# Kernel optimization log

Measured on AMD Instinct MI355X. Metric: run time of the kernel, lower is better.

The kernel has to match this reference:

```python
import jax, jax.numpy as jnp
import numpy as np
from jax import lax

SIGMA = 1.0
SIGMA_CUTOFF = 2.0
TAU = 1.0
EPS = 1e-6


def _gauss_kernel1d(sigma=SIGMA, cutoff=SIGMA_CUTOFF):
    r = int(round(cutoff * sigma))
    x = np.arange(-r, r + 1, dtype=np.float32)
    k = np.exp(-(x ** 2) / (2.0 * sigma ** 2))
    return jnp.asarray(k / k.sum())


def _smooth3d(x, k1d):
    # x: [1, 3, D, H, W]; separable depthwise Gaussian along each spatial axis
    k = k1d.shape[0]
    for axis in range(3):
        shape = [1, 1, 1]
        shape[axis] = k
        w = jnp.broadcast_to(k1d.reshape(shape), (3, 1) + tuple(shape))  # [3,1,kd,kh,kw]
        x = lax.conv_general_dilated(
            x, w, window_strides=(1, 1, 1), padding='SAME',
            feature_group_count=3,
            dimension_numbers=('NCDHW', 'OIDHW', 'NCDHW'))
    return x


def setup_inputs() -> dict:
    key = jax.random.key(0)
    k1, k2 = jax.random.split(key)
    shape = (1, 1, 128, 160, 160)
    moving_image = jax.random.normal(k1, shape, dtype=jnp.float32)
    fixed_image = jax.random.normal(k2, shape, dtype=jnp.float32)
    return {"moving_image": moving_image, "fixed_image": fixed_image, "iterations": 10}


def reference(moving_image, fixed_image, iterations):
    mov = moving_image[0, 0]  # [D,H,W]
    fix = fixed_image[0, 0]
    D, H, W = mov.shape
    dtype = mov.dtype
    grid = jnp.stack(jnp.meshgrid(
        jnp.arange(D, dtype=dtype),
        jnp.arange(H, dtype=dtype),
        jnp.arange(W, dtype=dtype), indexing='ij'))  # [3,D,H,W]
    grad_fixed = jnp.stack(jnp.gradient(fix))  # [3,D,H,W] (passive gradient, precomputed)
    k1d = _gauss_kernel1d()

    def warp(vf):
        coords = grid + vf
        return jax.scipy.ndimage.map_coordinates(
            mov, [coords[0], coords[1], coords[2]], order=1, mode='constant', cval=0.0)

    def step(vf, _):
        warped = warp(vf)                      # trilinear spatial transformer
        diff = warped - fix                    # intensity difference
        grad_warped = jnp.stack(jnp.gradient(warped))
        g = grad_warped + grad_fixed           # 'dual' demons gradient
        denom = jnp.sum(g * g, axis=0) + diff * diff
        scale = jnp.where(denom > EPS, -diff / denom, 0.0)  # demon force magnitude
        forces = scale[None] * g               # [3,D,H,W]
        vf = vf + TAU * forces                 # vector-field update
        vf = _smooth3d(vf[None], k1d)[0]       # Gaussian regularization
        return vf, None

    vf0 = jnp.zeros((3, D, H, W), dtype=dtype)
    vf, _ = lax.scan(step, vf0, None, length=iterations)
    return vf[None]  # [1,3,D,H,W]
```

## Files before the change

kernel.cpp:

```cpp
#include <hip/hip_runtime.h>
#include <math.h>

#define D_ 128
#define H_ 160
#define W_ 160
#define NVOX (D_*H_*W_)
#define HW (H_*W_)
#define N4 (NVOX/4)
#define HW4 (HW/4)

#define K0 0.40261996f
#define K1 0.24420134f
#define K2 0.05448868f

union F4 { float4 v; float a[4]; };

__device__ __forceinline__ float4 zero4() { float4 z; z.x=z.y=z.z=z.w=0.f; return z; }
__device__ __forceinline__ float4 bcast4(float x) { float4 r; r.x=r.y=r.z=r.w=x; return r; }

#define GLOAD_LDS16(g, l) __builtin_amdgcn_global_load_lds( \
    (const __attribute__((address_space(1))) void*)(g), \
    (__attribute__((address_space(3))) void*)(l), 16, 0, 0)

__device__ __forceinline__ float fetch_mov(const float* __restrict__ m, int d, int h, int w) {
    if ((unsigned)d >= (unsigned)D_ || (unsigned)h >= (unsigned)H_ || (unsigned)w >= (unsigned)W_) return 0.0f;
    return m[(size_t)(d*H_ + h)*W_ + w];
}

__device__ __forceinline__ float trilerp(const float* __restrict__ mov,
                                         float cd, float ch, float cw) {
    float fd = floorf(cd), fh = floorf(ch), fw = floorf(cw);
    int di = (int)fd, hi = (int)fh, wi = (int)fw;
    float td = cd - fd, th = ch - fh, tw = cw - fw;
    float c000, c001, c010, c011, c100, c101, c110, c111;
    if (di >= 0 && di < D_-1 && hi >= 0 && hi < H_-1 && wi >= 0 && wi < W_-1) {
        const float* p = mov + (size_t)di*HW + hi*W_ + wi;
        c000 = p[0];    c001 = p[1];
        c010 = p[W_];   c011 = p[W_+1];
        const float* q = p + HW;
        c100 = q[0];    c101 = q[1];
        c110 = q[W_];   c111 = q[W_+1];
    } else {
        c000 = fetch_mov(mov, di,   hi,   wi  );
        c001 = fetch_mov(mov, di,   hi,   wi+1);
        c010 = fetch_mov(mov, di,   hi+1, wi  );
        c011 = fetch_mov(mov, di,   hi+1, wi+1);
        c100 = fetch_mov(mov, di+1, hi,   wi  );
        c101 = fetch_mov(mov, di+1, hi,   wi+1);
        c110 = fetch_mov(mov, di+1, hi+1, wi  );
        c111 = fetch_mov(mov, di+1, hi+1, wi+1);
    }
    float c00 = c000 + tw*(c001 - c000);
    float c01 = c010 + tw*(c011 - c010);
    float c10 = c100 + tw*(c101 - c100);
    float c11 = c110 + tw*(c111 - c110);
    float c0 = c00 + th*(c01 - c00);
    float c1 = c10 + th*(c11 - c10);
    return c0 + td*(c1 - c0);
}

#define UROW 48

__global__ __launch_bounds__(256, 4) void force_wh_kernel(const float* __restrict__ warped,
                                                          const float* __restrict__ fix,
                                                          const float* __restrict__ vf,
                                                          float* __restrict__ tout,
                                                          int zero_vf) {
    __shared__ float u[3][36][UROW];
    __shared__ float tw[38][48];
    __shared__ float tf[38][48];
    const int tx = threadIdx.x;
    const int ty = threadIdx.y;
    const int tid = ty*8 + tx;
    const int bswz = (blockIdx.x & 7)*400 + (blockIdx.x >> 3);
    const int d   = bswz / 25;
    const int rem = bswz % 25;
    const int h0 = (rem / 5) * 32;
    const int w0 = (rem % 5) * 32;

    #define UF4(ch, r, fc) (((float4*)&u[(ch)][(r)][0]) + ((fc) ^ ((r)&3)))

    {
        const float* wplane = warped + (size_t)d*HW;
        const float* fplane = fix    + (size_t)d*HW;
        #pragma unroll
        for (int k = 0; k < 2; ++k) {
            int s = (k == 0) ? tid : 200 + tid;
            int R  = s / 12, C4 = s % 12;
            int gh = h0 - 3 + R;
            int ghc = gh < 0 ? 0 : (gh > H_-1 ? H_-1 : gh);
            int gw = w0 - 8 + 4*C4;
            int gwc = gw < 0 ? 0 : (gw > W_-4 ? W_-4 : gw);
            const float* ws2 = wplane + (size_t)ghc*W_ + gwc;
            const float* fs2 = fplane + (size_t)ghc*W_ + gwc;
            GLOAD_LDS16(ws2, ((float4*)tw) + s);
            GLOAD_LDS16(fs2, ((float4*)tf) + s);
        }
    }
    __syncthreads();
    if (w0 == 0 || w0 == 128) {
        if (tid < 152) {
            int vol = tid / 76;
            int t2  = tid % 76;
            int R = t2 / 2, C = t2 % 2;
            float (*tp)[48] = vol ? tf : tw;
            int dstc = (w0 == 0) ? C : (10 + C);
            int srcf = (w0 == 0) ? 8 : 39;
            float v = tp[R][srcf];
            *(float4*)&tp[R][4*dstc] = bcast4(v);
        }
        __syncthreads();
    }

    for (int slot = tid; slot < 360; slot += 256) {
        int r = slot/10, c = slot%10;
        int gh = h0 - 2 + r;
        int gw = w0 - 4 + 4*c;
        F4 o0, o1, o2;
        if ((unsigned)gh < (unsigned)H_ && gw >= 0 && gw + 4 <= W_) {
            size_t base = (size_t)d*HW + (size_t)gh*W_ + gw;
            int i4 = (int)(base >> 2);
            int up = (d < D_-1) ?  (HW/4) : 0;
            int dn = (d > 0)    ? -(HW/4) : 0;
            const float4* w4p = (const float4*)warped;
            const float4* f4p = (const float4*)fix;
            F4 du, dnv, fdu, fdn;
            du.v  = w4p[i4 + up];
            dnv.v = w4p[i4 + dn];
            fdu.v = f4p[i4 + up];
            fdn.v = f4p[i4 + dn];
            if (zero_vf) {
                o0.v = zero4(); o1.v = zero4(); o2.v = zero4();
            } else {
                o0.v = ((const float4*)vf)[i4];
                o1.v = ((const float4*)vf)[i4 + N4];
                o2.v = ((const float4*)vf)[i4 + 2*N4];
            }
            int sr = r + 1, sc = 4*c + 4;
            F4 cc, fc, hu, hd, fhu, fhd;
            cc.v  = *(const float4*)&tw[sr  ][sc];
            fc.v  = *(const float4*)&tf[sr  ][sc];
            hu.v  = *(const float4*)&tw[sr+1][sc];
            hd.v  = *(const float4*)&tw[sr-1][sc];
            fhu.v = *(const float4*)&tf[sr+1][sc];
            fhd.v = *(const float4*)&tf[sr-1][sc];
            float cl = tw[sr][sc-1], cr = tw[sr][sc+4];
            float fl = tf[sr][sc-1], fr = tf[sr][sc+4];
            float hs  = (gh==0 || gh==H_-1) ? 1.f : 0.5f;
            float dsc = (d==0  || d==D_-1)  ? 1.f : 0.5f;
            float m [6] = {cl, cc.a[0], cc.a[1], cc.a[2], cc.a[3], cr};
            float fm[6] = {fl, fc.a[0], fc.a[1], fc.a[2], fc.a[3], fr};
            #pragma unroll
            for (int j = 0; j < 4; ++j) {
                int wj = gw + j;
                float wsc  = (wj == 0 || wj == W_-1) ? 1.f : 0.5f;
                float prev  = (wj == 0)    ? m[1]  : m[j];
                float next  = (wj == W_-1) ? m[4]  : m[j+2];
                float fprev = (wj == 0)    ? fm[1] : fm[j];
                float fnext = (wj == W_-1) ? fm[4] : fm[j+2];
                float G0 = dsc*(du.a[j] - dnv.a[j]) + dsc*(fdu.a[j] - fdn.a[j]);
                float G1 = hs *(hu.a[j] - hd.a[j])  + hs *(fhu.a[j] - fhd.a[j]);
                float G2 = wsc*(next - prev)        + wsc*(fnext - fprev);
                float diff = cc.a[j] - fc.a[j];
                float denom = G0*G0 + G1*G1 + G2*G2 + diff*diff;
                float scale = (denom > 1e-6f) ? (-diff/denom) : 0.0f;
                o0.a[j] += scale*G0;
                o1.a[j] += scale*G1;
                o2.a[j] += scale*G2;
            }
        } else {
            o0.v = zero4(); o1.v = zero4(); o2.v = zero4();
        }
        *UF4(0, r, c) = o0.v;
        *UF4(1, r, c) = o1.v;
        *UF4(2, r, c) = o2.v;
    }
    __syncthreads();

    F4 wout[4];
    int jch = 0, jr = 0, jh = 0;
    const bool has = (tid < 216);
    if (has) {
        jch = tid / 72;
        int rem2 = tid % 72;
        jr = rem2 >> 1;
        jh = rem2 & 1;
        F4 q[6];
        #pragma unroll
        for (int i = 0; i < 6; ++i) q[i].v = *UF4(jch, jr, 4*jh + i);
        float mm[24];
        #pragma unroll
        for (int i = 0; i < 6; ++i) {
            mm[4*i+0]=q[i].a[0]; mm[4*i+1]=q[i].a[1]; mm[4*i+2]=q[i].a[2]; mm[4*i+3]=q[i].a[3];
        }
        #pragma unroll
        for (int o = 0; o < 16; ++o)
            wout[o>>2].a[o&3] = K2*(mm[o+2]+mm[o+6]) + K1*(mm[o+3]+mm[o+5]) + K0*mm[o+4];
    }
    __syncthreads();

    if (has) {
        #pragma unroll
        for (int f = 0; f < 4; ++f) *UF4(jch, jr, 4*jh + f) = wout[f].v;
    }
    __syncthreads();

    size_t base = (size_t)d*HW + (h0+ty)*W_ + w0 + 4*tx;
    #pragma unroll
    for (int ch = 0; ch < 3; ++ch) {
        F4 q0, q1, q2, q3, q4;
        q0.v = *UF4(ch, ty  , tx);
        q1.v = *UF4(ch, ty+1, tx);
        q2.v = *UF4(ch, ty+2, tx);
        q3.v = *UF4(ch, ty+3, tx);
        q4.v = *UF4(ch, ty+4, tx);
        float4 s2;
        s2.x = K2*(q0.a[0]+q4.a[0]) + K1*(q1.a[0]+q3.a[0]) + K0*q2.a[0];
        s2.y = K2*(q0.a[1]+q4.a[1]) + K1*(q1.a[1]+q3.a[1]) + K0*q2.a[1];
        s2.z = K2*(q0.a[2]+q4.a[2]) + K1*(q1.a[2]+q3.a[2]) + K0*q2.a[2];
        s2.w = K2*(q0.a[3]+q4.a[3]) + K1*(q1.a[3]+q3.a[3]) + K0*q2.a[3];
        *(float4*)(tout + (size_t)ch*NVOX + base) = s2;
    }
    #undef UF4
}

__global__ __launch_bounds__(256) void smooth_d_warp_kernel(const float* __restrict__ t,
                                                            const float* __restrict__ mov,
                                                            float* __restrict__ vf_out,
                                                            float* __restrict__ warped_out,
                                                            int do_warp) {
    __shared__ float4 sm[24][64];
    const int chunk = (blockIdx.x & 7)*400 + (blockIdx.x >> 3);
    const int db = chunk / 100;
    const int hb = chunk % 100;
    const int tdx = threadIdx.x & 63;
    const int tdz = threadIdx.x >> 6;
    const int d0 = db*4;
    const int hw4 = hb*64 + tdx;

    #pragma unroll
    for (int i = 0; i < 6; ++i) {
        int pc = tdz*6 + i;
        int ch = pc >> 3;
        int r  = pc & 7;
        int p  = d0 - 2 + r;
        if ((unsigned)p < (unsigned)D_) {
            const float4* src = (const float4*)(t + (size_t)ch*NVOX) + (p*HW4 + hw4);
            GLOAD_LDS16(src, &sm[pc][tdx]);
        } else {
            sm[pc][tdx] = zero4();
        }
    }
    __syncthreads();

    const int d = d0 + tdz;
    const int w = (hw4 % (W_/4)) * 4;
    const int h = hw4 / (W_/4);
    F4 va[3];
    #pragma unroll
    for (int ch = 0; ch < 3; ++ch) {
        F4 q0, q1, q2, q3, q4;
        q0.v = sm[ch*8 + tdz    ][tdx];
        q1.v = sm[ch*8 + tdz + 1][tdx];
        q2.v = sm[ch*8 + tdz + 2][tdx];
        q3.v = sm[ch*8 + tdz + 3][tdx];
        q4.v = sm[ch*8 + tdz + 4][tdx];
        va[ch].a[0] = K2*(q0.a[0]+q4.a[0]) + K1*(q1.a[0]+q3.a[0]) + K0*q2.a[0];
        va[ch].a[1] = K2*(q0.a[1]+q4.a[1]) + K1*(q1.a[1]+q3.a[1]) + K0*q2.a[1];
        va[ch].a[2] = K2*(q0.a[2]+q4.a[2]) + K1*(q1.a[2]+q3.a[2]) + K0*q2.a[2];
        va[ch].a[3] = K2*(q0.a[3]+q4.a[3]) + K1*(q1.a[3]+q3.a[3]) + K0*q2.a[3];
    }
    const int i4 = d*HW4 + hw4;
    ((float4*)vf_out)[i4]        = va[0].v;
    ((float4*)vf_out)[i4 + N4]   = va[1].v;
    ((float4*)vf_out)[i4 + 2*N4] = va[2].v;
    if (do_warp) {
        F4 r4o;
        #pragma unroll
        for (int j = 0; j < 4; ++j) {
            float cd  = (float)d       + va[0].a[j];
            float ch2 = (float)h       + va[1].a[j];
            float cw  = (float)(w + j) + va[2].a[j];
            r4o.a[j] = trilerp(mov, cd, ch2, cw);
        }
        ((float4*)warped_out)[i4] = r4o.v;
    }
}

extern "C" void kernel_launch(void* const* d_in, const int* in_sizes, int n_in,
                              void* d_out, int out_size, void* d_ws, size_t ws_size,
                              hipStream_t stream) {
    const float* mov = (const float*)d_in[0];
    const float* fix = (const float*)d_in[1];
    const int ITERS = 10;

    float* ws     = (float*)d_ws;
    float* vfA    = ws;
    float* tbuf   = ws + (size_t)3*NVOX;
    float* warped = ws + (size_t)6*NVOX;

    for (int it = 0; it < ITERS; ++it) {
        const float* wsrc = (it == 0) ? mov : warped;
        force_wh_kernel<<<dim3(3200), dim3(8,32), 0, stream>>>(wsrc, fix, vfA, tbuf,
                                                               it == 0 ? 1 : 0);
        float* vdst = (it == ITERS-1) ? (float*)d_out : vfA;
        smooth_d_warp_kernel<<<dim3(3200), dim3(256), 0, stream>>>(tbuf, mov, vdst, warped,
                                                                   it == ITERS-1 ? 0 : 1);
    }
}
```

Before: 538.5 us.

## Precompute warped+fixed sum and difference volumes to halve force-kernel reads

Since the dual demons gradient is linear, grad(warped)+grad(fix) equals grad(warped+fix). The warp kernel now writes S=warped+fix and D=warped-fix instead of the warped volume, and a prep kernel builds them once for the first iteration. The force kernel then stages one LDS tile instead of two and makes fewer global loads, and its occupancy hint is raised from 4 to 5. In exchange the warp kernel reads fix and writes two volumes instead of one, and the workspace grows by one volume.

After: 535.7 us. About the same (-0.5%).

```diff
diff --git a/kernel.cpp b/kernel.cpp
--- a/kernel.cpp
+++ b/kernel.cpp
@@ -59,16 +59,30 @@
     return c0 + td*(c1 - c0);
 }
 
+__global__ __launch_bounds__(256) void prep_kernel(const float* __restrict__ mov,
+                                                   const float* __restrict__ fix,
+                                                   float* __restrict__ S,
+                                                   float* __restrict__ DIF) {
+    int i4 = blockIdx.x*256 + threadIdx.x;
+    if (i4 >= N4) return;
+    F4 m4; m4.v = ((const float4*)mov)[i4];
+    F4 f4; f4.v = ((const float4*)fix)[i4];
+    F4 s4, d4;
+    #pragma unroll
+    for (int j = 0; j < 4; ++j) { s4.a[j] = m4.a[j] + f4.a[j]; d4.a[j] = m4.a[j] - f4.a[j]; }
+    ((float4*)S)[i4]   = s4.v;
+    ((float4*)DIF)[i4] = d4.v;
+}
+
 #define UROW 48
 
-__global__ __launch_bounds__(256, 4) void force_wh_kernel(const float* __restrict__ warped,
-                                                          const float* __restrict__ fix,
+__global__ __launch_bounds__(256, 5) void force_wh_kernel(const float* __restrict__ S,
+                                                          const float* __restrict__ DIF,
                                                           const float* __restrict__ vf,
                                                           float* __restrict__ tout,
                                                           int zero_vf) {
     __shared__ float u[3][36][UROW];
-    __shared__ float tw[38][48];
-    __shared__ float tf[38][48];
+    __shared__ float ts[38][48];
     const int tx = threadIdx.x;
     const int ty = threadIdx.y;
     const int tid = ty*8 + tx;
@@ -81,8 +95,7 @@
     #define UF4(ch, r, fc) (((float4*)&u[(ch)][(r)][0]) + ((fc) ^ ((r)&3)))
 
     {
-        const float* wplane = warped + (size_t)d*HW;
-        const float* fplane = fix    + (size_t)d*HW;
+        const float* splane = S + (size_t)d*HW;
         #pragma unroll
         for (int k = 0; k < 2; ++k) {
             int s = (k == 0) ? tid : 200 + tid;
@@ -91,23 +104,17 @@
             int ghc = gh < 0 ? 0 : (gh > H_-1 ? H_-1 : gh);
             int gw = w0 - 8 + 4*C4;
             int gwc = gw < 0 ? 0 : (gw > W_-4 ? W_-4 : gw);
-            const float* ws2 = wplane + (size_t)ghc*W_ + gwc;
-            const float* fs2 = fplane + (size_t)ghc*W_ + gwc;
-            GLOAD_LDS16(ws2, ((float4*)tw) + s);
-            GLOAD_LDS16(fs2, ((float4*)tf) + s);
+            GLOAD_LDS16(splane + (size_t)ghc*W_ + gwc, ((float4*)ts) + s);
         }
     }
     __syncthreads();
     if (w0 == 0 || w0 == 128) {
-        if (tid < 152) {
-            int vol = tid / 76;
-            int t2  = tid % 76;
-            int R = t2 / 2, C = t2 % 2;
-            float (*tp)[48] = vol ? tf : tw;
+        if (tid < 76) {
+            int R = tid / 2, C = tid % 2;
             int dstc = (w0 == 0) ? C : (10 + C);
             int srcf = (w0 == 0) ? 8 : 39;
-            float v = tp[R][srcf];
-            *(float4*)&tp[R][4*dstc] = bcast4(v);
+            float v = ts[R][srcf];
+            *(float4*)&ts[R][4*dstc] = bcast4(v);
         }
         __syncthreads();
     }
@@ -122,13 +129,11 @@
             int i4 = (int)(base >> 2);
             int up = (d < D_-1) ?  (HW/4) : 0;
             int dn = (d > 0)    ? -(HW/4) : 0;
-            const float4* w4p = (const float4*)warped;
-            const float4* f4p = (const float4*)fix;
-            F4 du, dnv, fdu, fdn;
-            du.v  = w4p[i4 + up];
-            dnv.v = w4p[i4 + dn];
-            fdu.v = f4p[i4 + up];
-            fdn.v = f4p[i4 + dn];
+            const float4* S4 = (const float4*)S;
+            F4 sdu, sdn, dff;
+            sdu.v = S4[i4 + up];
+            sdn.v = S4[i4 + dn];
+            dff.v = ((const float4*)DIF)[i4];
             if (zero_vf) {
                 o0.v = zero4(); o1.v = zero4(); o2.v = zero4();
             } else {
@@ -137,31 +142,24 @@
                 o2.v = ((const float4*)vf)[i4 + 2*N4];
             }
             int sr = r + 1, sc = 4*c + 4;
-            F4 cc, fc, hu, hd, fhu, fhd;
-            cc.v  = *(const float4*)&tw[sr  ][sc];
-            fc.v  = *(const float4*)&tf[sr  ][sc];
-            hu.v  = *(const float4*)&tw[sr+1][sc];
-            hd.v  = *(const float4*)&tw[sr-1][sc];
-            fhu.v = *(const float4*)&tf[sr+1][sc];
-            fhd.v = *(const float4*)&tf[sr-1][sc];
-            float cl = tw[sr][sc-1], cr = tw[sr][sc+4];
-            float fl = tf[sr][sc-1], fr = tf[sr][sc+4];
+            F4 scc, shu, shd;
+            scc.v = *(const float4*)&ts[sr  ][sc];
+            shu.v = *(const float4*)&ts[sr+1][sc];
+            shd.v = *(const float4*)&ts[sr-1][sc];
+            float sl = ts[sr][sc-1], sr2 = ts[sr][sc+4];
             float hs  = (gh==0 || gh==H_-1) ? 1.f : 0.5f;
             float dsc = (d==0  || d==D_-1)  ? 1.f : 0.5f;
-            float m [6] = {cl, cc.a[0], cc.a[1], cc.a[2], cc.a[3], cr};
-            float fm[6] = {fl, fc.a[0], fc.a[1], fc.a[2], fc.a[3], fr};
+            float m[6] = {sl, scc.a[0], scc.a[1], scc.a[2], scc.a[3], sr2};
             #pragma unroll
             for (int j = 0; j < 4; ++j) {
                 int wj = gw + j;
                 float wsc  = (wj == 0 || wj == W_-1) ? 1.f : 0.5f;
-                float prev  = (wj == 0)    ? m[1]  : m[j];
-                float next  = (wj == W_-1) ? m[4]  : m[j+2];
-                float fprev = (wj == 0)    ? fm[1] : fm[j];
-                float fnext = (wj == W_-1) ? fm[4] : fm[j+2];
-                float G0 = dsc*(du.a[j] - dnv.a[j]) + dsc*(fdu.a[j] - fdn.a[j]);
-                float G1 = hs *(hu.a[j] - hd.a[j])  + hs *(fhu.a[j] - fhd.a[j]);
-                float G2 = wsc*(next - prev)        + wsc*(fnext - fprev);
-                float diff = cc.a[j] - fc.a[j];
+                float prev = (wj == 0)    ? m[1] : m[j];
+                float next = (wj == W_-1) ? m[4] : m[j+2];
+                float G0 = dsc*(sdu.a[j] - sdn.a[j]);
+                float G1 = hs *(shu.a[j] - shd.a[j]);
+                float G2 = wsc*(next - prev);
+                float diff = dff.a[j];
                 float denom = G0*G0 + G1*G1 + G2*G2 + diff*diff;
                 float scale = (denom > 1e-6f) ? (-diff/denom) : 0.0f;
                 o0.a[j] += scale*G0;
@@ -226,8 +224,10 @@
 
 __global__ __launch_bounds__(256) void smooth_d_warp_kernel(const float* __restrict__ t,
                                                             const float* __restrict__ mov,
+                                                            const float* __restrict__ fix,
                                                             float* __restrict__ vf_out,
-                                                            float* __restrict__ warped_out,
+                                                            float* __restrict__ S_out,
+                                                            float* __restrict__ D_out,
                                                             int do_warp) {
     __shared__ float4 sm[24][64];
     const int chunk = (blockIdx.x & 7)*400 + (blockIdx.x >> 3);
@@ -283,7 +283,15 @@
             float cw  = (float)(w + j) + va[2].a[j];
             r4o.a[j] = trilerp(mov, cd, ch2, cw);
         }
-        ((float4*)warped_out)[i4] = r4o.v;
+        F4 fx; fx.v = ((const float4*)fix)[i4];
+        F4 s4o, d4o;
+        #pragma unroll
+        for (int j = 0; j < 4; ++j) {
+            s4o.a[j] = r4o.a[j] + fx.a[j];
+            d4o.a[j] = r4o.a[j] - fx.a[j];
+        }
+        ((float4*)S_out)[i4] = s4o.v;
+        ((float4*)D_out)[i4] = d4o.v;
     }
 }
 
@@ -297,14 +305,17 @@
     float* ws     = (float*)d_ws;
     float* vfA    = ws;
     float* tbuf   = ws + (size_t)3*NVOX;
-    float* warped = ws + (size_t)6*NVOX;
+    float* Svol   = ws + (size_t)6*NVOX;
+    float* Dvol   = ws + (size_t)7*NVOX;
+
+    prep_kernel<<<dim3(3200), dim3(256), 0, stream>>>(mov, fix, Svol, Dvol);
 
     for (int it = 0; it < ITERS; ++it) {
-        const float* wsrc = (it == 0) ? mov : warped;
-        force_wh_kernel<<<dim3(3200), dim3(8,32), 0, stream>>>(wsrc, fix, vfA, tbuf,
+        force_wh_kernel<<<dim3(3200), dim3(8,32), 0, stream>>>(Svol, Dvol, vfA, tbuf,
                                                                it == 0 ? 1 : 0);
         float* vdst = (it == ITERS-1) ? (float*)d_out : vfA;
-        smooth_d_warp_kernel<<<dim3(3200), dim3(256), 0, stream>>>(tbuf, mov, vdst, warped,
+        smooth_d_warp_kernel<<<dim3(3200), dim3(256), 0, stream>>>(tbuf, mov, fix, vdst,
+                                                                   Svol, Dvol,
                                                                    it == ITERS-1 ? 0 : 1);
     }
 }
```
